# Kernel tuning notes

Hardware: AMD Instinct MI355X
Metric: run time of the kernel (lower is better)

Reference implementation:

```python
import jax, jax.numpy as jnp
import numpy as np

B, N, J, F, C = 8, 2048, 4, 16, 2

def setup_inputs() -> dict:
    key = jax.random.key(0)
    k1, k2, k3, k4 = jax.random.split(key, 4)
    W = jax.random.normal(k1, (B, N, N, J), dtype=jnp.float32)
    x = jax.random.normal(k2, (B, F, N, 1), dtype=jnp.float32)
    # Conv2d(F*J, C, 1) weight [C, F*J, 1, 1] -> flattened [C, F*J], plus bias [C]
    conv_w = jax.random.normal(k3, (C, F * J), dtype=jnp.float32) / np.sqrt(F * J)
    conv_b = jax.random.normal(k4, (C,), dtype=jnp.float32) * 0.01
    return {"W": W, "x": x, "conv_w": conv_w, "conv_b": conv_b}

def reference(W, x, conv_w, conv_b):
    b, n, _, j = W.shape
    f = x.shape[1]
    # gmul: out[b, j*F+f, n] = sum_m x[b,f,m] * W[b,m,n,j]
    y = jnp.einsum('bfm,bmnj->bjfn', x[..., 0], W).reshape(b, j * f, n)
    # 1x1 conv over the (J*F) channel dim
    out = jnp.einsum('ck,bkn->bcn', conv_w, y) + conv_b[None, :, None]
    # squeeze(3).transpose(1,2) -> [B, N, C] (squeeze(2) is a no-op for C=2)
    return out.transpose(0, 2, 1)
```

## Files before the change

### kernel.cpp

```cpp
#include <hip/hip_runtime.h>
#include <hip/hip_bf16.h>

constexpr int B = 8, N = 2048, J = 4, F = 16, C = 2;
constexpr int MS = 16;
constexpr int MC = N / MS;
constexpr int TN = 256;
constexpr int NT = N / TN;

__global__ __launch_bounds__(256) void gnn_fused_kernel(
    const float* __restrict__ W,
    const float* __restrict__ x,
    const float* __restrict__ cw,
    const float* __restrict__ cb,
    float* __restrict__ out)
{
    __shared__ float t[MC][8];
    __shared__ float s_cw[C * J * F];

    const int tid = threadIdx.x;
    const int blk = blockIdx.x;
    const int mchunk = blk % MS;
    const int tmp    = blk / MS;
    const int ntile  = tmp % NT;
    const int b      = tmp / NT;
    const int m0 = mchunk * MC;
    const int n0 = ntile * TN;

    if (tid < C * J * F) s_cw[tid] = cw[tid];
    __syncthreads();

    if (tid < MC) {
        const int m = m0 + tid;
        const float* xb = x + (size_t)b * F * N + m;
        float xv[F];
#pragma unroll
        for (int f = 0; f < F; ++f) xv[f] = xb[(size_t)f * N];
#pragma unroll
        for (int c = 0; c < C; ++c) {
#pragma unroll
            for (int j = 0; j < J; ++j) {
                float s = 0.f;
#pragma unroll
                for (int f = 0; f < F; ++f) s += s_cw[c * (J * F) + j * F + f] * xv[f];
                t[tid][c * 4 + j] = s;
            }
        }
    }
    __syncthreads();

    const int n = n0 + tid;
    const float4* Wp = (const float4*)(W + (((size_t)b * N + m0) * N + n) * J);
    const size_t mstride = (size_t)N * J / 4;

    float acc0 = 0.f, acc1 = 0.f;
#pragma unroll 4
    for (int mi = 0; mi < MC; ++mi) {
        float4 w4 = Wp[(size_t)mi * mstride];
        const float4* tv = (const float4*)t[mi];
        float4 t0 = tv[0];
        float4 t1 = tv[1];
        acc0 += w4.x * t0.x + w4.y * t0.y + w4.z * t0.z + w4.w * t0.w;
        acc1 += w4.x * t1.x + w4.y * t1.y + w4.z * t1.z + w4.w * t1.w;
    }

    if (mchunk == 0) { acc0 += cb[0]; acc1 += cb[1]; }

    float* o = out + ((size_t)b * N + n) * C;
    atomicAdd(o,     acc0);
    atomicAdd(o + 1, acc1);
}

extern "C" void kernel_launch(void* const* d_in, const int* in_sizes, int n_in,
                              void* d_out, int out_size, void* d_ws, size_t ws_size,
                              hipStream_t stream) {
    const float* W  = (const float*)d_in[0];
    const float* x  = (const float*)d_in[1];
    const float* cw = (const float*)d_in[2];
    const float* cb = (const float*)d_in[3];
    float* out = (float*)d_out;

    hipMemsetAsync(out, 0, (size_t)out_size * sizeof(float), stream);

    dim3 grid(B * NT * MS);
    dim3 block(TN);
    gnn_fused_kernel<<<grid, block, 0, stream>>>(W, x, cw, cb, out);
}
```

Measured before the change: 98.65 us.

## Split t precompute into prep kernel and reduce m-chunks in shared memory

Moves the conv-weight-times-x precompute into a separate prep kernel that writes to the workspace. The main kernel now has each 512-thread block cover 32 columns across all m, splitting m over 16 sub-groups. It reduces through shared memory and writes the output directly, dropping the memset and global atomics. W is read with nontemporal loads, and each block stages the full per-batch t vector (64KB) in LDS. This removes redundant t recomputation and atomic traffic, but each block's W row reads are now only 512B wide, and the large LDS footprint may limit occupancy.

```diff
diff --git a/kernel.cpp b/kernel.cpp
--- a/kernel.cpp
+++ b/kernel.cpp
@@ -2,72 +2,103 @@
 #include <hip/hip_bf16.h>
 
 constexpr int B = 8, N = 2048, J = 4, F = 16, C = 2;
-constexpr int MS = 16;
-constexpr int MC = N / MS;
-constexpr int TN = 256;
-constexpr int NT = N / TN;
 
-__global__ __launch_bounds__(256) void gnn_fused_kernel(
-    const float* __restrict__ W,
+typedef float fx4 __attribute__((ext_vector_type(4)));
+
+__global__ __launch_bounds__(256) void gnn_prep_kernel(
     const float* __restrict__ x,
     const float* __restrict__ cw,
+    float* __restrict__ t_ws)
+{
+    __shared__ float s_cw[C * J * F];
+    const int tid = threadIdx.x;
+    if (tid < C * J * F) s_cw[tid] = cw[tid];
+    __syncthreads();
+
+    const int gid = blockIdx.x * 256 + tid;
+    const int b = gid >> 11;
+    const int m = gid & (N - 1);
+
+    const float* xb = x + (size_t)b * F * N + m;
+    float xv[F];
+#pragma unroll
+    for (int f = 0; f < F; ++f) xv[f] = xb[(size_t)f * N];
+
+    float t8[8];
+#pragma unroll
+    for (int c = 0; c < C; ++c) {
+#pragma unroll
+        for (int j = 0; j < J; ++j) {
+            float s = 0.f;
+#pragma unroll
+            for (int f = 0; f < F; ++f) s += s_cw[c * (J * F) + j * F + f] * xv[f];
+            t8[c * 4 + j] = s;
+        }
+    }
+    float4* dst = (float4*)(t_ws + (size_t)gid * 8);
+    dst[0] = *(float4*)&t8[0];
+    dst[1] = *(float4*)&t8[4];
+}
+
+constexpr int TN = 32;
+constexpr int NT = N / TN;
+constexpr int BT = 512;
+constexpr int MSUB = 16;
+constexpr int MC = N / MSUB;
+
+__global__ __launch_bounds__(512) void gnn_main_kernel(
+    const float* __restrict__ W,
+    const float* __restrict__ t_ws,
     const float* __restrict__ cb,
     float* __restrict__ out)
 {
-    __shared__ float t[MC][8];
-    __shared__ float s_cw[C * J * F];
+    __shared__ float tl[N * 8];
+    __shared__ float red[MSUB][TN][C];
 
     const int tid = threadIdx.x;
     const int blk = blockIdx.x;
-    const int mchunk = blk % MS;
-    const int tmp    = blk / MS;
-    const int ntile  = tmp % NT;
-    const int b      = tmp / NT;
-    const int m0 = mchunk * MC;
+    const int b = blk >> 6;
+    const int ntile = blk & (NT - 1);
     const int n0 = ntile * TN;
 
-    if (tid < C * J * F) s_cw[tid] = cw[tid];
-    __syncthreads();
-
-    if (tid < MC) {
-        const int m = m0 + tid;
-        const float* xb = x + (size_t)b * F * N + m;
-        float xv[F];
+    {
+        const float4* src = (const float4*)(t_ws + (size_t)b * N * 8);
+        float4* dst = (float4*)tl;
 #pragma unroll
-        for (int f = 0; f < F; ++f) xv[f] = xb[(size_t)f * N];
-#pragma unroll
-        for (int c = 0; c < C; ++c) {
-#pragma unroll
-            for (int j = 0; j < J; ++j) {
-                float s = 0.f;
-#pragma unroll
-                for (int f = 0; f < F; ++f) s += s_cw[c * (J * F) + j * F + f] * xv[f];
-                t[tid][c * 4 + j] = s;
-            }
-        }
+        for (int i = 0; i < (N * 8 / 4) / BT; ++i)
+            dst[i * BT + tid] = src[i * BT + tid];
     }
     __syncthreads();
 
-    const int n = n0 + tid;
-    const float4* Wp = (const float4*)(W + (((size_t)b * N + m0) * N + n) * J);
-    const size_t mstride = (size_t)N * J / 4;
+    const int nl = tid & (TN - 1);
+    const int msub = tid >> 5;
+    const int m0 = msub * MC;
+
+    const fx4* Wp = (const fx4*)W + (((size_t)b * N + m0) * N + n0 + nl);
 
     float acc0 = 0.f, acc1 = 0.f;
-#pragma unroll 4
+#pragma unroll 8
     for (int mi = 0; mi < MC; ++mi) {
-        float4 w4 = Wp[(size_t)mi * mstride];
-        const float4* tv = (const float4*)t[mi];
+        fx4 w4 = __builtin_nontemporal_load(Wp + (size_t)mi * N);
+        const float4* tv = (const float4*)&tl[(m0 + mi) * 8];
         float4 t0 = tv[0];
         float4 t1 = tv[1];
         acc0 += w4.x * t0.x + w4.y * t0.y + w4.z * t0.z + w4.w * t0.w;
         acc1 += w4.x * t1.x + w4.y * t1.y + w4.z * t1.z + w4.w * t1.w;
     }
 
-    if (mchunk == 0) { acc0 += cb[0]; acc1 += cb[1]; }
+    red[msub][nl][0] = acc0;
+    red[msub][nl][1] = acc1;
+    __syncthreads();
 
-    float* o = out + ((size_t)b * N + n) * C;
-    atomicAdd(o,     acc0);
-    atomicAdd(o + 1, acc1);
+    if (tid < TN * C) {
+        const int nl2 = tid >> 1;
+        const int c = tid & 1;
+        float s = cb[c];
+#pragma unroll
+        for (int k = 0; k < MSUB; ++k) s += red[k][nl2][c];
+        out[((size_t)b * N + n0 + nl2) * C + c] = s;
+    }
 }
 
 extern "C" void kernel_launch(void* const* d_in, const int* in_sizes, int n_in,
@@ -77,11 +108,9 @@
     const float* x  = (const float*)d_in[1];
     const float* cw = (const float*)d_in[2];
     const float* cb = (const float*)d_in[3];
-    float* out = (float*)d_out;
+    float* out  = (float*)d_out;
+    float* t_ws = (float*)d_ws;
 
-    hipMemsetAsync(out, 0, (size_t)out_size * sizeof(float), stream);
-
-    dim3 grid(B * NT * MS);
-    dim3 block(TN);
-    gnn_fused_kernel<<<grid, block, 0, stream>>>(W, x, cw, cb, out);
+    gnn_prep_kernel<<<dim3(B * N / 256), dim3(256), 0, stream>>>(x, cw, t_ws);
+    gnn_main_kernel<<<dim3(B * NT), dim3(BT), 0, stream>>>(W, t_ws, cb, out);
 }
```

After: 100.5 us. Within noise of the previous version (+1.8%).

## Replace output atomics with partial buffers and last-block reduction, nontemporal W loads

Applied to the files above, without the earlier changes.

Each block now handles 512 output columns across a 128-row m-chunk and writes its partial sums to a workspace buffer instead of issuing atomicAdds on the output. A per-group counter picks the last-arriving block, which sums the 16 partials, adds the bias and writes the output with one vectorized store. This removes the need to zero the output before launch. W is streamed with nontemporal loads to avoid polluting the cache, and the block/grid shape changes from 256 to 512 threads. The kernel is mostly bound by reading W, so the benefit depends on how much the atomics and cache behavior were costing. The extra partial-buffer traffic and the tail work in the last block add some overhead.

```diff
diff --git a/kernel.cpp b/kernel.cpp
--- a/kernel.cpp
+++ b/kernel.cpp
@@ -2,36 +2,42 @@
 #include <hip/hip_bf16.h>
 
 constexpr int B = 8, N = 2048, J = 4, F = 16, C = 2;
-constexpr int MS = 16;
-constexpr int MC = N / MS;
-constexpr int TN = 256;
-constexpr int NT = N / TN;
+constexpr int MCH = 16;
+constexpr int MR  = N / MCH;
+constexpr int NH  = 4;
+constexpr int HN  = N / NH;
+constexpr int NGROUP = B * NH;
+constexpr int GRID = NGROUP * MCH;
 
-__global__ __launch_bounds__(256) void gnn_fused_kernel(
+typedef float fx4 __attribute__((ext_vector_type(4)));
+
+__global__ __launch_bounds__(512) void gnn_main_kernel(
     const float* __restrict__ W,
     const float* __restrict__ x,
     const float* __restrict__ cw,
     const float* __restrict__ cb,
+    float* __restrict__ part,
+    int* __restrict__ ctr,
     float* __restrict__ out)
 {
-    __shared__ float t[MC][8];
     __shared__ float s_cw[C * J * F];
+    __shared__ float tl[MR * 8];
+    __shared__ int isLast;
 
     const int tid = threadIdx.x;
     const int blk = blockIdx.x;
-    const int mchunk = blk % MS;
-    const int tmp    = blk / MS;
-    const int ntile  = tmp % NT;
-    const int b      = tmp / NT;
-    const int m0 = mchunk * MC;
-    const int n0 = ntile * TN;
+    const int g  = blk >> 4;
+    const int mc = blk & (MCH - 1);
+    const int b  = g >> 2;
+    const int nh = g & (NH - 1);
+    const int m0 = mc * MR;
+    const int n0 = nh * HN;
 
     if (tid < C * J * F) s_cw[tid] = cw[tid];
     __syncthreads();
 
-    if (tid < MC) {
-        const int m = m0 + tid;
-        const float* xb = x + (size_t)b * F * N + m;
+    if (tid < MR) {
+        const float* xb = x + (size_t)b * F * N + m0 + tid;
         float xv[F];
 #pragma unroll
         for (int f = 0; f < F; ++f) xv[f] = xb[(size_t)f * N];
@@ -42,32 +48,49 @@
                 float s = 0.f;
 #pragma unroll
                 for (int f = 0; f < F; ++f) s += s_cw[c * (J * F) + j * F + f] * xv[f];
-                t[tid][c * 4 + j] = s;
+                tl[tid * 8 + c * 4 + j] = s;
             }
         }
     }
     __syncthreads();
 
-    const int n = n0 + tid;
-    const float4* Wp = (const float4*)(W + (((size_t)b * N + m0) * N + n) * J);
-    const size_t mstride = (size_t)N * J / 4;
+    const fx4* Wp = (const fx4*)W + ((size_t)b * N + m0) * N + n0;
 
     float acc0 = 0.f, acc1 = 0.f;
 #pragma unroll 4
-    for (int mi = 0; mi < MC; ++mi) {
-        float4 w4 = Wp[(size_t)mi * mstride];
-        const float4* tv = (const float4*)t[mi];
-        float4 t0 = tv[0];
-        float4 t1 = tv[1];
+    for (int r = 0; r < MR; ++r) {
+        const float4 t0 = *(const float4*)&tl[r * 8];
+        const float4 t1 = *(const float4*)&tl[r * 8 + 4];
+        fx4 w4 = __builtin_nontemporal_load(Wp + (size_t)r * N + tid);
         acc0 += w4.x * t0.x + w4.y * t0.y + w4.z * t0.z + w4.w * t0.w;
         acc1 += w4.x * t1.x + w4.y * t1.y + w4.z * t1.z + w4.w * t1.w;
     }
 
-    if (mchunk == 0) { acc0 += cb[0]; acc1 += cb[1]; }
+    float* pb = part + ((size_t)(g * MCH + mc) * C) * HN;
+    pb[tid]      = acc0;
+    pb[HN + tid] = acc1;
 
-    float* o = out + ((size_t)b * N + n) * C;
-    atomicAdd(o,     acc0);
-    atomicAdd(o + 1, acc1);
+    __threadfence();
+    __syncthreads();
+    if (tid == 0) {
+        int old = __hip_atomic_fetch_add(&ctr[g], 1, __ATOMIC_ACQ_REL,
+                                         __HIP_MEMORY_SCOPE_AGENT);
+        isLast = (old == MCH - 1);
+    }
+    __syncthreads();
+
+    if (isLast) {
+        __threadfence();
+        const float* pg = part + (size_t)g * MCH * C * HN;
+        float s0 = cb[0], s1 = cb[1];
+#pragma unroll 8
+        for (int m = 0; m < MCH; ++m) {
+            s0 += pg[(size_t)(m * C + 0) * HN + tid];
+            s1 += pg[(size_t)(m * C + 1) * HN + tid];
+        }
+        float2 ov; ov.x = s0; ov.y = s1;
+        *(float2*)&out[(size_t)(b * N + n0 + tid) * C] = ov;
+    }
 }
 
 extern "C" void kernel_launch(void* const* d_in, const int* in_sizes, int n_in,
@@ -77,11 +100,10 @@
     const float* x  = (const float*)d_in[1];
     const float* cw = (const float*)d_in[2];
     const float* cb = (const float*)d_in[3];
-    float* out = (float*)d_out;
+    float* out  = (float*)d_out;
+    float* part = (float*)d_ws;
+    int*   ctr  = (int*)(part + (size_t)NGROUP * MCH * C * HN);
 
-    hipMemsetAsync(out, 0, (size_t)out_size * sizeof(float), stream);
-
-    dim3 grid(B * NT * MS);
-    dim3 block(TN);
-    gnn_fused_kernel<<<grid, block, 0, stream>>>(W, x, cw, cb, out);
+    hipMemsetAsync(ctr, 0, NGROUP * sizeof(int), stream);
+    gnn_main_kernel<<<dim3(GRID), dim3(512), 0, stream>>>(W, x, cw, cb, part, ctr, out);
 }
```

Measured after the change: 266.9 us. 171% more time.
